# Performance work log

Measured on AMD Instinct MI355X. Metric: run time of the kernel, lower is better.

Reference implementation:

```python
import jax, jax.numpy as jnp
import numpy as np

B = 2048


def _maxpool2(x):
    return jax.lax.reduce_window(x, -jnp.inf, jax.lax.max,
                                 (1, 1, 2, 2), (1, 1, 2, 2), 'VALID')


def setup_inputs() -> dict:
    key = jax.random.key(0)
    ks = jax.random.split(key, 7)
    return {
        'x': jax.random.normal(ks[0], (B, 3, 32, 32), dtype=jnp.float32),
        'conv_w': jax.random.normal(ks[1], (45, 1, 5, 5), dtype=jnp.float32),
        'conv_b': jax.random.normal(ks[2], (45,), dtype=jnp.float32) * 0.1,
        'tree_w': jax.random.normal(ks[3], (1, 16, 15, 3, 7, 7, 2, 2), dtype=jnp.float32),
        'tree_b': jax.random.normal(ks[4], (1, 16, 3, 7), dtype=jnp.float32),
        'fc_w': jax.random.normal(ks[5], (10, 336), dtype=jnp.float32),
        'fc_b': jax.random.normal(ks[6], (10,), dtype=jnp.float32) * 0.1,
    }


def reference(x, conv_w, conv_b, tree_w, tree_b, fc_w, fc_b):
    # grouped conv: in=3, groups=3, out=45, kernel 5x5, VALID -> (B,45,28,28)
    out = jax.lax.conv_general_dilated(
        x, conv_w, window_strides=(1, 1), padding='VALID',
        dimension_numbers=('NCHW', 'OIHW', 'NCHW'), feature_group_count=3)
    out = jax.nn.sigmoid(out + conv_b[None, :, None, None])
    out = _maxpool2(out)  # (B,45,14,14)
    b = out.shape[0]
    # unfold((2,2),stride=2) + the torch reshape/transpose chain is equivalent to:
    # (B,45,14,14) -> (b, g=3, m=15, i=7, ki=2, j=7, kj=2) -> (b,m,g,i,j,ki,kj)
    xt = out.reshape(b, 3, 15, 7, 2, 7, 2).transpose(0, 2, 1, 3, 5, 4, 6)
    # TreeLayer: elementwise mul with weights (16,m,g,i,j,ki,kj) then sum over m,j,ki,kj
    t = jnp.einsum('bmgijkl,fmgijkl->bfgi', xt, tree_w[0]) + tree_b  # (B,16,3,7)
    t = jax.nn.sigmoid(t)
    return t.reshape(b, 16 * 3 * 7) @ fc_w.T + fc_b  # (B,10)
```

## Files before the change

kernel.cpp:

```cpp
#include <hip/hip_runtime.h>
#include <hip/hip_fp16.h>

#define BATCH 2048

typedef _Float16 f16x8 __attribute__((ext_vector_type(8)));
typedef float f32x4 __attribute__((ext_vector_type(4)));

#define XROW 18
#define XPL  584
#define XIMG 1168
#define PIS  3152

__device__ __forceinline__ float fast_sigmoid(float v) {
    return __builtin_amdgcn_rcpf(1.0f + __builtin_amdgcn_exp2f(v * -1.44269504f));
}

#define WS_W3B  0
#define WS_FCW  301056

__global__ __launch_bounds__(256) void k_prep(
    const float* __restrict__ tree_w,
    const float* __restrict__ fc_w,
    ushort* __restrict__ W3B,
    float* __restrict__ FCW2,
    float* __restrict__ out)
{
    int pidx = blockIdx.x * 256 + threadIdx.x;
    if (pidx < 35280) {
        float4 v = ((const float4*)tree_w)[pidx];
        int j  = pidx % 7;
        int t1 = pidx / 7;
        int i  = t1 % 7;
        int t2 = t1 / 7;
        int g  = t2 % 3;
        int t3 = t2 / 3;
        int nn = t3 % 15;
        int f  = t3 / 15;
        int gi = g * 7 + i;
        int u  = nn & 7;
        int hi = nn >> 3;
        float vv[4] = {v.x, v.y, v.z, v.w};
        #pragma unroll
        for (int e = 0; e < 4; e++) {
            int ki = e >> 1, kj = e & 1;
            int u27 = ki * 14 + j * 2 + kj;
            int c   = u27 >> 1;
            int qq  = (u27 & 1) * 2 + hi;
            W3B[(size_t)(gi * 14 + c) * 512 + (qq * 16 + f) * 8 + u] =
                __half_as_ushort(__float2half(vv[e]));
        }
    } else if (pidx < 38640) {
        int jj = pidx - 35280;
        int f = jj & 15;
        int r = jj >> 4;
        int i = r % 7;
        int r2 = r / 7;
        int o = r2 % 10;
        int g = r2 / 10;
        FCW2[jj] = fc_w[o * 336 + f * 21 + g * 7 + i];
    } else if (pidx < 48048) {
        int z = pidx - 38640;
        int f  = z & 15;
        int qq = ((z >> 4) & 1) * 2 + 1;
        int r  = z >> 5;
        int c  = r % 14;
        int gi = r / 14;
        W3B[(size_t)(gi * 14 + c) * 512 + (qq * 16 + f) * 8 + 7] = 0;
    } else if (pidx < 68528) {
        out[pidx - 48048] = 0.f;
    }
}

__global__ __launch_bounds__(256, 4) void kF_all(
    const float* __restrict__ x,
    const float* __restrict__ conv_w,
    const float* __restrict__ conv_b,
    const ushort* __restrict__ W3B,
    const float* __restrict__ FCW2,
    const float* __restrict__ tree_b,
    const float* __restrict__ fc_b,
    float* __restrict__ out)
{
    __shared__ __align__(16) unsigned xsc[2 * XIMG];
    __shared__ __align__(16) ushort ps[4 * PIS];
    ushort* tsl = (ushort*)xsc;

    const int tid  = threadIdx.x;
    const int blk  = blockIdx.x;
    const int quad = blk / 3;
    const int g    = blk - quad * 3;
    const int img0 = quad * 4;
    const int lane = tid & 63;
    const int n    = lane & 15;
    const int q    = lane >> 4;
    const int wave = tid >> 6;

    float4 xv[4];
    #pragma unroll
    for (int im = 0; im < 4; im++)
        xv[im] = ((const float4*)(x + (size_t)(img0 + im) * 3072 + g * 1024))[tid];

    if (tid < 128) {
        int im = tid >> 6, pl = (tid >> 5) & 1, row = tid & 31;
        *(uint2*)&xsc[im * XIMG + pl * XPL + row * XROW + 16] = make_uint2(0u, 0u);
    }

    f16x8 B1 = {0, 0, 0, 0, 0, 0, 0, 0};
    f16x8 B2 = {0, 0, 0, 0, 0, 0, 0, 0};
    float bs = 0.f;
    if (n < 15) {
        const float* wrow = conv_w + (g * 15 + n) * 25;
        #pragma unroll
        for (int u = 0; u < 5; u++) B1[u] = (_Float16)wrow[q * 5 + u];
        if (q == 0) {
            #pragma unroll
            for (int u = 0; u < 5; u++) B2[u] = (_Float16)wrow[20 + u];
        }
        bs = conv_b[g * 15 + n] * -1.44269504f;
    }

    const int dr = (n >> 1) & 1, dc = n & 1, n4 = n >> 2;
    const int a2cd = (4 - q) * XROW;
    int aoffd[13];
    {
        int pb = wave * 4 + n4;
        int ph = (pb >= 14) ? 1 : 0;
        int pw = pb - 14 * ph;
        int base = dc * XPL + (dr + q) * XROW;
        #pragma unroll
        for (int it = 0; it < 13; it++) {
            aoffd[it] = base + 2 * ph * XROW + pw;
            pw += 2; ph += 1;
            if (pw >= 14) { pw -= 14; ph += 1; }
        }
    }

    const int prow = tid >> 3, pt = tid & 7;
    auto pack_img = [&](int im2, float4 v) {
        __half2 a = __float22half2_rn(make_float2(v.x, v.y));
        __half2 b = __float22half2_rn(make_float2(v.z, v.w));
        unsigned d0 = *(unsigned*)&a, d1 = *(unsigned*)&b;
        unsigned n0 = (unsigned)__shfl_down((int)d0, 1);
        if (pt == 7) n0 = 0u;
        unsigned t01 = (d0 >> 16) | (d1 << 16);
        unsigned t12 = (d1 >> 16) | (n0 << 16);
        unsigned* base = xsc + im2 * XIMG + prow * XROW + 2 * pt;
        *(uint2*)(base)       = make_uint2(d0, d1);
        *(uint2*)(base + XPL) = make_uint2(t01, t12);
    };

    auto conv_tile2 = [&](int it, ushort* pso) {
        const unsigned* p0 = xsc + aoffd[it];
        const unsigned* p1 = p0 + XIMG;
        union U { unsigned w[4]; f16x8 v; };
        U A1a, A2a, A1b, A2b;
        #pragma unroll
        for (int e = 0; e < 4; e++) {
            A1a.w[e] = p0[e];
            A2a.w[e] = p0[a2cd + e];
            A1b.w[e] = p1[e];
            A2b.w[e] = p1[a2cd + e];
        }
        f32x4 da = {0.f, 0.f, 0.f, 0.f}, db = {0.f, 0.f, 0.f, 0.f};
        da = __builtin_amdgcn_mfma_f32_16x16x32_f16(A1a.v, B1, da, 0, 0, 0);
        db = __builtin_amdgcn_mfma_f32_16x16x32_f16(A1b.v, B1, db, 0, 0, 0);
        da = __builtin_amdgcn_mfma_f32_16x16x32_f16(A2a.v, B2, da, 0, 0, 0);
        db = __builtin_amdgcn_mfma_f32_16x16x32_f16(A2b.v, B2, db, 0, 0, 0);
        float mxa = fmaxf(fmaxf(da[0], da[1]), fmaxf(da[2], da[3]));
        float mxb = fmaxf(fmaxf(db[0], db[1]), fmaxf(db[2], db[3]));
        float ea = __builtin_amdgcn_exp2f(fmaf(mxa, -1.44269504f, bs));
        float eb = __builtin_amdgcn_exp2f(fmaf(mxb, -1.44269504f, bs));
        int so = (wave + it * 4) * 64 + lane;
        pso[so] =
            __half_as_ushort(__float2half(__builtin_amdgcn_rcpf(1.0f + ea)));
        pso[PIS + so] =
            __half_as_ushort(__float2half(__builtin_amdgcn_rcpf(1.0f + eb)));
    };

    #pragma unroll
    for (int r2 = 0; r2 < 2; r2++) {
        pack_img(0, xv[r2 * 2 + 0]);
        pack_img(1, xv[r2 * 2 + 1]);
        __syncthreads();

        ushort* pso = ps + (r2 * 2) * PIS;
        #pragma unroll
        for (int it = 0; it < 12; it++) conv_tile2(it, pso);
        if (wave == 0) conv_tile2(12, pso);
        __syncthreads();
    }

    for (int ii = wave; ii < 7; ii += 4) {
        const f16x8* Wb = (const f16x8*)W3B + (size_t)(g * 7 + ii) * 896;
        const ushort* ap = ps + (n & 3) * PIS + ii * 448;
        f16x8 Bf[14];
        #pragma unroll
        for (int c = 0; c < 14; c++) Bf[c] = Wb[c * 64 + lane];
        f32x4 D0 = {0.f, 0.f, 0.f, 0.f};
        f32x4 D1 = {0.f, 0.f, 0.f, 0.f};
        #pragma unroll
        for (int c = 0; c < 7; c++) {
            f16x8 Ae = *(const f16x8*)(ap + (2 * c) * 32 + q * 8);
            D0 = __builtin_amdgcn_mfma_f32_16x16x32_f16(Ae, Bf[2 * c], D0, 0, 0, 0);
            f16x8 Ao = *(const f16x8*)(ap + (2 * c + 1) * 32 + q * 8);
            D1 = __builtin_amdgcn_mfma_f32_16x16x32_f16(Ao, Bf[2 * c + 1], D1, 0, 0, 0);
        }
        if (q == 0) {
            float tb = tree_b[n * 21 + g * 7 + ii];
            #pragma unroll
            for (int im = 0; im < 4; im++) {
                float t = (D0[im] + D1[im]) + tb;
                tsl[(im * 7 + ii) * 16 + n] =
                    __half_as_ushort(__float2half(fast_sigmoid(t)));
            }
        }
    }
    __syncthreads();

    if (lane < 10) {
        const int im4 = wave, o = lane;
        const uint2* tp = (const uint2*)(tsl + im4 * 112);
        const float4* wp = (const float4*)(FCW2 + (size_t)(g * 10 + o) * 112);
        float acc = (g == 0) ? fc_b[o] : 0.f;
        #pragma unroll
        for (int jj = 0; jj < 28; jj++) {
            float4 w4 = wp[jj];
            uint2 hv = tp[jj];
            float2 p0 = __half22float2(*(const __half2*)&hv.x);
            float2 p1 = __half22float2(*(const __half2*)&hv.y);
            acc = fmaf(p0.x, w4.x, acc);
            acc = fmaf(p0.y, w4.y, acc);
            acc = fmaf(p1.x, w4.z, acc);
            acc = fmaf(p1.y, w4.w, acc);
        }
#if defined(__HIP_PLATFORM_AMD__)
        unsafeAtomicAdd(out + (size_t)(img0 + im4) * 10 + o, acc);
#else
        atomicAdd(out + (size_t)(img0 + im4) * 10 + o, acc);
#endif
    }
}

extern "C" void kernel_launch(void* const* d_in, const int* in_sizes, int n_in,
                              void* d_out, int out_size, void* d_ws, size_t ws_size,
                              hipStream_t stream) {
    const float* x      = (const float*)d_in[0];
    const float* conv_w = (const float*)d_in[1];
    const float* conv_b = (const float*)d_in[2];
    const float* tree_w = (const float*)d_in[3];
    const float* tree_b = (const float*)d_in[4];
    const float* fc_w   = (const float*)d_in[5];
    const float* fc_b   = (const float*)d_in[6];
    float* out = (float*)d_out;

    ushort* W3B  = (ushort*)((char*)d_ws + WS_W3B);
    float*  FCW2 = (float*)((char*)d_ws + WS_FCW);

    k_prep<<<268, 256, 0, stream>>>(tree_w, fc_w, W3B, FCW2, out);
    kF_all<<<512 * 3, 256, 0, stream>>>(x, conv_w, conv_b, W3B, FCW2,
                                        tree_b, fc_b, out);
}
```

Measured before the change: 102.3 us.

## Prefetch tree weights during conv, shrink LDS row pitch, skip redundant second-tap loads

The LDS row stride for the packed input drops from 18 to 17 words, which shrinks the scratch footprint and changes the bank mapping. The second conv MFMA operand is now loaded only by quad 0, and the other quads keep a zeroed register instead of reading padding. The first tree-weight fragment load is issued before the second conv pass so its global latency overlaps with the conv compute, and the tree GEMM becomes a lambda called explicitly per wave. The risks are higher register pressure from the hoisted Bf[14] array and the odd stride causing misaligned access patterns.

```diff
diff --git a/kernel.cpp b/kernel.cpp
--- a/kernel.cpp
+++ b/kernel.cpp
@@ -6,9 +6,9 @@
 typedef _Float16 f16x8 __attribute__((ext_vector_type(8)));
 typedef float f32x4 __attribute__((ext_vector_type(4)));
 
-#define XROW 18
-#define XPL  584
-#define XIMG 1168
+#define XROW 17
+#define XPL  552
+#define XIMG 1104
 #define PIS  3152
 
 __device__ __forceinline__ float fast_sigmoid(float v) {
@@ -102,7 +102,7 @@
 
     if (tid < 128) {
         int im = tid >> 6, pl = (tid >> 5) & 1, row = tid & 31;
-        *(uint2*)&xsc[im * XIMG + pl * XPL + row * XROW + 16] = make_uint2(0u, 0u);
+        xsc[im * XIMG + pl * XPL + row * XROW + 16] = 0u;
     }
 
     f16x8 B1 = {0, 0, 0, 0, 0, 0, 0, 0};
@@ -120,7 +120,6 @@
     }
 
     const int dr = (n >> 1) & 1, dc = n & 1, n4 = n >> 2;
-    const int a2cd = (4 - q) * XROW;
     int aoffd[13];
     {
         int pb = wave * 4 + n4;
@@ -149,17 +148,26 @@
         *(uint2*)(base + XPL) = make_uint2(t01, t12);
     };
 
+    union U { unsigned w[4]; f16x8 v; };
+    U A2a, A2b;
+    #pragma unroll
+    for (int e = 0; e < 4; e++) { A2a.w[e] = 0u; A2b.w[e] = 0u; }
+
     auto conv_tile2 = [&](int it, ushort* pso) {
         const unsigned* p0 = xsc + aoffd[it];
         const unsigned* p1 = p0 + XIMG;
-        union U { unsigned w[4]; f16x8 v; };
-        U A1a, A2a, A1b, A2b;
+        U A1a, A1b;
         #pragma unroll
         for (int e = 0; e < 4; e++) {
             A1a.w[e] = p0[e];
-            A2a.w[e] = p0[a2cd + e];
             A1b.w[e] = p1[e];
-            A2b.w[e] = p1[a2cd + e];
+        }
+        if (q == 0) {
+            #pragma unroll
+            for (int e = 0; e < 4; e++) {
+                A2a.w[e] = p0[68 + e];
+                A2b.w[e] = p1[68 + e];
+            }
         }
         f32x4 da = {0.f, 0.f, 0.f, 0.f}, db = {0.f, 0.f, 0.f, 0.f};
         da = __builtin_amdgcn_mfma_f32_16x16x32_f16(A1a.v, B1, da, 0, 0, 0);
@@ -177,25 +185,9 @@
             __half_as_ushort(__float2half(__builtin_amdgcn_rcpf(1.0f + eb)));
     };
 
-    #pragma unroll
-    for (int r2 = 0; r2 < 2; r2++) {
-        pack_img(0, xv[r2 * 2 + 0]);
-        pack_img(1, xv[r2 * 2 + 1]);
-        __syncthreads();
-
-        ushort* pso = ps + (r2 * 2) * PIS;
-        #pragma unroll
-        for (int it = 0; it < 12; it++) conv_tile2(it, pso);
-        if (wave == 0) conv_tile2(12, pso);
-        __syncthreads();
-    }
-
-    for (int ii = wave; ii < 7; ii += 4) {
-        const f16x8* Wb = (const f16x8*)W3B + (size_t)(g * 7 + ii) * 896;
+    f16x8 Bf[14];
+    auto tree_gemm = [&](int ii) {
         const ushort* ap = ps + (n & 3) * PIS + ii * 448;
-        f16x8 Bf[14];
-        #pragma unroll
-        for (int c = 0; c < 14; c++) Bf[c] = Wb[c * 64 + lane];
         f32x4 D0 = {0.f, 0.f, 0.f, 0.f};
         f32x4 D1 = {0.f, 0.f, 0.f, 0.f};
         #pragma unroll
@@ -214,6 +206,35 @@
                     __half_as_ushort(__float2half(fast_sigmoid(t)));
             }
         }
+    };
+
+    pack_img(0, xv[0]);
+    pack_img(1, xv[1]);
+    __syncthreads();
+    #pragma unroll
+    for (int it = 0; it < 12; it++) conv_tile2(it, ps);
+    if (wave == 0) conv_tile2(12, ps);
+    __syncthreads();
+
+    pack_img(0, xv[2]);
+    pack_img(1, xv[3]);
+    __syncthreads();
+    {
+        const f16x8* Wb = (const f16x8*)W3B + (size_t)(g * 7 + wave) * 896;
+        #pragma unroll
+        for (int c = 0; c < 14; c++) Bf[c] = Wb[c * 64 + lane];
+    }
+    #pragma unroll
+    for (int it = 0; it < 12; it++) conv_tile2(it, ps + 2 * PIS);
+    if (wave == 0) conv_tile2(12, ps + 2 * PIS);
+    __syncthreads();
+
+    tree_gemm(wave);
+    if (wave < 3) {
+        const f16x8* Wb = (const f16x8*)W3B + (size_t)(g * 7 + wave + 4) * 896;
+        #pragma unroll
+        for (int c = 0; c < 14; c++) Bf[c] = Wb[c * 64 + lane];
+        tree_gemm(wave + 4);
     }
     __syncthreads();
 
```

New measurement: 108.7 us. 1.06x slower.

## Repack conv input into four shifted planes and prefetch tree weights earlier

Applied to the files above, without the earlier changes.

Shared-memory staging of the input image changes from two column-shifted planes of 32-bit words to four 16-bit planes shifted by 0 to 3 columns. Each conv A-fragment can then be read as two aligned 8-byte loads instead of four scalar loads. Images are now processed one at a time (four pack/conv rounds instead of two paired rounds). The first tree-weight fragment load is issued during the last conv round so its global latency overlaps the conv work. The cost is more LDS writes per pack, two extra barriers, and higher register pressure from holding Bf across the conv loop.

```diff
diff --git a/kernel.cpp b/kernel.cpp
--- a/kernel.cpp
+++ b/kernel.cpp
@@ -6,10 +6,9 @@
 typedef _Float16 f16x8 __attribute__((ext_vector_type(8)));
 typedef float f32x4 __attribute__((ext_vector_type(4)));
 
-#define XROW 18
-#define XPL  584
-#define XIMG 1168
-#define PIS  3152
+#define RST 36
+#define CST 1168
+#define PIS 3152
 
 __device__ __forceinline__ float fast_sigmoid(float v) {
     return __builtin_amdgcn_rcpf(1.0f + __builtin_amdgcn_exp2f(v * -1.44269504f));
@@ -81,9 +80,9 @@
     const float* __restrict__ fc_b,
     float* __restrict__ out)
 {
-    __shared__ __align__(16) unsigned xsc[2 * XIMG];
+    __shared__ __align__(16) ushort xsc[4 * CST];
     __shared__ __align__(16) ushort ps[4 * PIS];
-    ushort* tsl = (ushort*)xsc;
+    ushort* tsl = xsc;
 
     const int tid  = threadIdx.x;
     const int blk  = blockIdx.x;
@@ -100,11 +99,6 @@
     for (int im = 0; im < 4; im++)
         xv[im] = ((const float4*)(x + (size_t)(img0 + im) * 3072 + g * 1024))[tid];
 
-    if (tid < 128) {
-        int im = tid >> 6, pl = (tid >> 5) & 1, row = tid & 31;
-        *(uint2*)&xsc[im * XIMG + pl * XPL + row * XROW + 16] = make_uint2(0u, 0u);
-    }
-
     f16x8 B1 = {0, 0, 0, 0, 0, 0, 0, 0};
     f16x8 B2 = {0, 0, 0, 0, 0, 0, 0, 0};
     float bs = 0.f;
@@ -120,82 +114,77 @@
     }
 
     const int dr = (n >> 1) & 1, dc = n & 1, n4 = n >> 2;
-    const int a2cd = (4 - q) * XROW;
-    int aoffd[13];
+    const int a2c = (4 - q) * RST;
+    int aoff[13];
     {
         int pb = wave * 4 + n4;
         int ph = (pb >= 14) ? 1 : 0;
         int pw = pb - 14 * ph;
-        int base = dc * XPL + (dr + q) * XROW;
+        const int rbase = (dr + q) * RST;
         #pragma unroll
         for (int it = 0; it < 13; it++) {
-            aoffd[it] = base + 2 * ph * XROW + pw;
+            int s = 2 * (pw & 1) + dc;
+            aoff[it] = s * CST + rbase + 2 * ph * RST + 4 * (pw >> 1);
             pw += 2; ph += 1;
             if (pw >= 14) { pw -= 14; ph += 1; }
         }
     }
 
     const int prow = tid >> 3, pt = tid & 7;
-    auto pack_img = [&](int im2, float4 v) {
+    ushort* const pbase = xsc + prow * RST + pt * 4;
+    auto pack_img = [&](float4 v) {
         __half2 a = __float22half2_rn(make_float2(v.x, v.y));
         __half2 b = __float22half2_rn(make_float2(v.z, v.w));
         unsigned d0 = *(unsigned*)&a, d1 = *(unsigned*)&b;
         unsigned n0 = (unsigned)__shfl_down((int)d0, 1);
-        if (pt == 7) n0 = 0u;
+        unsigned n1 = (unsigned)__shfl_down((int)d1, 1);
+        if (pt == 7) { n0 = 0u; n1 = 0u; }
         unsigned t01 = (d0 >> 16) | (d1 << 16);
         unsigned t12 = (d1 >> 16) | (n0 << 16);
-        unsigned* base = xsc + im2 * XIMG + prow * XROW + 2 * pt;
-        *(uint2*)(base)       = make_uint2(d0, d1);
-        *(uint2*)(base + XPL) = make_uint2(t01, t12);
+        unsigned t23 = (n0 >> 16) | (n1 << 16);
+        *(uint2*)(pbase)           = make_uint2(d0, d1);
+        *(uint2*)(pbase + CST)     = make_uint2(t01, t12);
+        *(uint2*)(pbase + 2 * CST) = make_uint2(d1, n0);
+        *(uint2*)(pbase + 3 * CST) = make_uint2(t12, t23);
     };
 
-    auto conv_tile2 = [&](int it, ushort* pso) {
-        const unsigned* p0 = xsc + aoffd[it];
-        const unsigned* p1 = p0 + XIMG;
-        union U { unsigned w[4]; f16x8 v; };
-        U A1a, A2a, A1b, A2b;
-        #pragma unroll
-        for (int e = 0; e < 4; e++) {
-            A1a.w[e] = p0[e];
-            A2a.w[e] = p0[a2cd + e];
-            A1b.w[e] = p1[e];
-            A2b.w[e] = p1[a2cd + e];
-        }
-        f32x4 da = {0.f, 0.f, 0.f, 0.f}, db = {0.f, 0.f, 0.f, 0.f};
-        da = __builtin_amdgcn_mfma_f32_16x16x32_f16(A1a.v, B1, da, 0, 0, 0);
-        db = __builtin_amdgcn_mfma_f32_16x16x32_f16(A1b.v, B1, db, 0, 0, 0);
-        da = __builtin_amdgcn_mfma_f32_16x16x32_f16(A2a.v, B2, da, 0, 0, 0);
-        db = __builtin_amdgcn_mfma_f32_16x16x32_f16(A2b.v, B2, db, 0, 0, 0);
-        float mxa = fmaxf(fmaxf(da[0], da[1]), fmaxf(da[2], da[3]));
-        float mxb = fmaxf(fmaxf(db[0], db[1]), fmaxf(db[2], db[3]));
-        float ea = __builtin_amdgcn_exp2f(fmaf(mxa, -1.44269504f, bs));
-        float eb = __builtin_amdgcn_exp2f(fmaf(mxb, -1.44269504f, bs));
-        int so = (wave + it * 4) * 64 + lane;
-        pso[so] =
-            __half_as_ushort(__float2half(__builtin_amdgcn_rcpf(1.0f + ea)));
-        pso[PIS + so] =
-            __half_as_ushort(__float2half(__builtin_amdgcn_rcpf(1.0f + eb)));
+    auto conv_tile = [&](int it, ushort* pso) {
+        const ushort* pA = xsc + aoff[it];
+        union U { struct { uint2 a, b; } u; f16x8 v; };
+        U A1, A2;
+        A1.u.a = *(const uint2*)pA;
+        A1.u.b = *(const uint2*)(pA + 4);
+        A2.u.a = *(const uint2*)(pA + a2c);
+        A2.u.b = *(const uint2*)(pA + a2c + 4);
+        f32x4 d = {0.f, 0.f, 0.f, 0.f};
+        d = __builtin_amdgcn_mfma_f32_16x16x32_f16(A1.v, B1, d, 0, 0, 0);
+        d = __builtin_amdgcn_mfma_f32_16x16x32_f16(A2.v, B2, d, 0, 0, 0);
+        float mx = fmaxf(fmaxf(d[0], d[1]), fmaxf(d[2], d[3]));
+        float e = __builtin_amdgcn_exp2f(fmaf(mx, -1.44269504f, bs));
+        pso[(wave + it * 4) * 64 + lane] =
+            __half_as_ushort(__float2half(__builtin_amdgcn_rcpf(1.0f + e)));
     };
 
+    f16x8 Bf[14];
+
     #pragma unroll
-    for (int r2 = 0; r2 < 2; r2++) {
-        pack_img(0, xv[r2 * 2 + 0]);
-        pack_img(1, xv[r2 * 2 + 1]);
+    for (int rr = 0; rr < 4; rr++) {
+        pack_img(xv[rr]);
         __syncthreads();
-
-        ushort* pso = ps + (r2 * 2) * PIS;
-        #pragma unroll
-        for (int it = 0; it < 12; it++) conv_tile2(it, pso);
-        if (wave == 0) conv_tile2(12, pso);
+        if (rr == 3) {
+            const f16x8* Wb = (const f16x8*)W3B + (size_t)(g * 7 + wave) * 896;
+            #pragma unroll
+            for (int c = 0; c < 14; c++) Bf[c] = Wb[c * 64 + lane];
+        }
+        ushort* pso = ps + rr * PIS;
+        #pragma unroll
+        for (int it = 0; it < 12; it++) conv_tile(it, pso);
+        if (wave == 0) conv_tile(12, pso);
         __syncthreads();
     }
 
-    for (int ii = wave; ii < 7; ii += 4) {
-        const f16x8* Wb = (const f16x8*)W3B + (size_t)(g * 7 + ii) * 896;
+    auto tree_gemm = [&](int ii) {
         const ushort* ap = ps + (n & 3) * PIS + ii * 448;
-        f16x8 Bf[14];
-        #pragma unroll
-        for (int c = 0; c < 14; c++) Bf[c] = Wb[c * 64 + lane];
         f32x4 D0 = {0.f, 0.f, 0.f, 0.f};
         f32x4 D1 = {0.f, 0.f, 0.f, 0.f};
         #pragma unroll
@@ -214,6 +203,14 @@
                     __half_as_ushort(__float2half(fast_sigmoid(t)));
             }
         }
+    };
+
+    tree_gemm(wave);
+    if (wave < 3) {
+        const f16x8* Wb = (const f16x8*)W3B + (size_t)(g * 7 + wave + 4) * 896;
+        #pragma unroll
+        for (int c = 0; c < 14; c++) Bf[c] = Wb[c * 64 + lane];
+        tree_gemm(wave + 4);
     }
     __syncthreads();
 
```

Result: slower. 109.5 us (+7.1%).
